# Kernel optimization log

Measured on AMD Instinct MI355X. Metric: run time of the kernel, lower is better.

## Reference

```python
import jax, jax.numpy as jnp
import numpy as np

REL_DIM = 64
HIDDEN = 128
IN_DIM = 7  # dist, dx, dy, color_diff(3), size_diff(1)


def setup_inputs() -> dict:
    key = jax.random.key(0)
    ks = jax.random.split(key, 8)
    B, N = 4, 512
    pos = jax.random.normal(ks[0], (B, N, 2), dtype=jnp.float32)
    color = jax.random.uniform(ks[1], (B, N, 3), dtype=jnp.float32)
    size = jax.random.uniform(ks[2], (B, N, 1), dtype=jnp.float32)
    # MLP params: Linear(7,128) -> GELU -> Linear(128,64), torch default init scale
    W1 = jax.random.normal(ks[3], (IN_DIM, HIDDEN), dtype=jnp.float32) / np.sqrt(IN_DIM)
    b1 = jax.random.normal(ks[4], (HIDDEN,), dtype=jnp.float32) * 0.01
    W2 = jax.random.normal(ks[5], (HIDDEN, REL_DIM), dtype=jnp.float32) / np.sqrt(HIDDEN)
    b2 = jax.random.normal(ks[6], (REL_DIM,), dtype=jnp.float32) * 0.01
    return {"pos": pos, "color": color, "size": size,
            "W1": W1, "b1": b1, "W2": W2, "b2": b2}


def reference(pos, color, size, W1, b1, W2, b2):
    # pos: (B,N,2), color: (B,N,3), size: (B,N,1)
    dx = pos[:, :, None, 0] - pos[:, None, :, 0]          # (B,N,N)
    dy = pos[:, :, None, 1] - pos[:, None, :, 1]          # (B,N,N)
    dist = jnp.sqrt(dx * dx + dy * dy + 1e-6)             # (B,N,N)
    color_diff = color[:, :, None, :] - color[:, None, :, :]  # (B,N,N,3)
    size_diff = size[:, :, None, :] - size[:, None, :, :]     # (B,N,N,1)
    geom = jnp.concatenate(
        [dist[..., None], dx[..., None], dy[..., None], color_diff, size_diff],
        axis=-1)                                          # (B,N,N,7)
    h = jax.nn.gelu(jnp.einsum('bijc,ch->bijh', geom, W1) + b1, approximate=False)
    rel = jnp.einsum('bijh,hr->bijr', h, W2) + b2          # (B,N,N,rel_dim)
    return rel
```

## Files before the change

kernel.cpp:

```cpp
#include <hip/hip_runtime.h>
#include <math.h>

#define NPTS 512
#define HID 128
#define RELD 64

typedef __attribute__((ext_vector_type(8))) short short8;
typedef __attribute__((ext_vector_type(4))) float f32x4;
typedef __attribute__((ext_vector_type(4))) int i32x4;

__global__ __launch_bounds__(256) void relgeom_mfma(
    const float* __restrict__ pos, const float* __restrict__ color,
    const float* __restrict__ size, const float* __restrict__ W1,
    const float* __restrict__ b1, const float* __restrict__ W2,
    const float* __restrict__ b2, float* __restrict__ out)
{
  __shared__ __align__(16) char lds[16384 + 4 * 4096];
  const int tid = threadIdx.x;
  const int lane = tid & 63;
  const int wid = tid >> 6;
  const int l15 = lane & 15, lq = lane >> 4, l3 = lane & 3;

#pragma unroll
  for (int n = 0; n < 32; ++n) {
    const int m = tid + 256 * n;
    const int k = m >> 6, r = m & 63;
    const __bf16 wb = (__bf16)W2[m];
    *(__bf16*)(lds + r * 256 + (((k >> 3) ^ (r & 7)) << 4) + (k & 7) * 2) = wb;
  }
  __syncthreads();

  const int pbase = (blockIdx.x * 4 + wid) * 64;
  const int t = pbase + lane;
  const int j = t & (NPTS - 1);
  const int bi = t >> 9;
  const int i = bi & (NPTS - 1);
  const int b = bi >> 9;
  const int pi = b * NPTS + i, pj = b * NPTS + j;

  const float dx = pos[pi * 2 + 0] - pos[pj * 2 + 0];
  const float dy = pos[pi * 2 + 1] - pos[pj * 2 + 1];
  const float g0 = sqrtf(fmaf(dx, dx, fmaf(dy, dy, 1e-6f)));
  const float g3 = color[pi * 3 + 0] - color[pj * 3 + 0];
  const float g4 = color[pi * 3 + 1] - color[pj * 3 + 1];
  const float g5 = color[pi * 3 + 2] - color[pj * 3 + 2];
  const float g6 = size[pi] - size[pj];

  f32x4 acc[4][4];
#pragma unroll
  for (int nt = 0; nt < 4; ++nt) {
    const float bb = b2[nt * 16 + l15];
#pragma unroll
    for (int s = 0; s < 4; ++s) acc[s][nt] = (f32x4){bb, bb, bb, bb};
  }

  char* const hbase = lds + 16384 + wid * 4096;

  for (int ks = 0; ks < 4; ++ks) {
    union { short s[32]; i32x4 v[4]; } hb;
#pragma unroll
    for (int kk = 0; kk < 32; ++kk) {
      const int k = ks * 32 + kk;
      float h = b1[k];
      h = fmaf(g0, W1[0 * HID + k], h);
      h = fmaf(dx, W1[1 * HID + k], h);
      h = fmaf(dy, W1[2 * HID + k], h);
      h = fmaf(g3, W1[3 * HID + k], h);
      h = fmaf(g4, W1[4 * HID + k], h);
      h = fmaf(g5, W1[5 * HID + k], h);
      h = fmaf(g6, W1[6 * HID + k], h);
      const float h2 = h * h;
      const float wq = fmaf(h2, -0.1029534f, -2.3022077f);
      const float ex = __builtin_amdgcn_exp2f(h * wq);
      const float gel = h * __builtin_amdgcn_rcpf(1.0f + ex);
      const __bf16 hbf = (__bf16)gel;
      hb.s[kk] = __builtin_bit_cast(short, hbf);
    }
#pragma unroll
    for (int d = 0; d < 4; ++d)
      *(i32x4*)(hbase + lane * 64 + ((d ^ l3) << 4)) = hb.v[d];

    short8 bfr[4];
#pragma unroll
    for (int nt = 0; nt < 4; ++nt) {
      const int r = nt * 16 + l15;
      bfr[nt] = *(const short8*)(lds + r * 256 + (((ks * 4 + lq) ^ (r & 7)) << 4));
    }
#pragma unroll
    for (int s = 0; s < 4; ++s) {
      const short8 af = *(const short8*)(hbase + (s * 16 + l15) * 64 + ((lq ^ l3) << 4));
#pragma unroll
      for (int nt = 0; nt < 4; ++nt)
        acc[s][nt] = __builtin_amdgcn_mfma_f32_16x16x32_bf16(af, bfr[nt], acc[s][nt], 0, 0, 0);
    }
  }

  float* const op = out + (size_t)pbase * RELD;
#pragma unroll
  for (int s = 0; s < 4; ++s)
#pragma unroll
    for (int nt = 0; nt < 4; ++nt)
#pragma unroll
      for (int ri = 0; ri < 4; ++ri)
        op[(s * 16 + lq * 4 + ri) * RELD + nt * 16 + l15] = acc[s][nt][ri];
}

extern "C" void kernel_launch(void* const* d_in, const int* in_sizes, int n_in,
                              void* d_out, int out_size, void* d_ws, size_t ws_size,
                              hipStream_t stream) {
  const float* pos   = (const float*)d_in[0];
  const float* color = (const float*)d_in[1];
  const float* size  = (const float*)d_in[2];
  const float* W1    = (const float*)d_in[3];
  const float* b1    = (const float*)d_in[4];
  const float* W2    = (const float*)d_in[5];
  const float* b2    = (const float*)d_in[6];
  float* out = (float*)d_out;

  const int B = in_sizes[0] / (NPTS * 2);
  const long long pairs = (long long)B * NPTS * NPTS;
  const int grid = (int)(pairs / 256);

  relgeom_mfma<<<grid, 256, 0, stream>>>(pos, color, size, W1, b1, W2, b2, out);
}
```

Baseline: 85.93 us.

## Factor first-layer linear terms into per-point tables precomputed in a prep kernel

The first linear layer is split algebraically: every term except the distance term is linear in per-point features, so per-point projections u_i (fp32 with bias) and u_j (bf16) are precomputed in a small prep kernel. The main kernel then forms each hidden pre-activation as u_i[k] - u_j[k] + dist*W1[0][k], which replaces seven FMAs per hidden unit with one FMA and a subtract. In exchange it adds a second launch, workspace use and per-pair table reads, and storing the u_j table in bf16 lowers precision. A fallback to the old kernel runs when the workspace is too small.

```diff
diff --git a/kernel.cpp b/kernel.cpp
--- a/kernel.cpp
+++ b/kernel.cpp
@@ -9,7 +9,121 @@
 typedef __attribute__((ext_vector_type(4))) float f32x4;
 typedef __attribute__((ext_vector_type(4))) int i32x4;
 
-__global__ __launch_bounds__(256) void relgeom_mfma(
+__global__ __launch_bounds__(256) void prep_tables(
+    const float* __restrict__ pos, const float* __restrict__ color,
+    const float* __restrict__ size, const float* __restrict__ W1,
+    const float* __restrict__ b1, float* __restrict__ ui,
+    unsigned short* __restrict__ uj)
+{
+  const int tid = blockIdx.x * blockDim.x + threadIdx.x;
+  const int k = tid & (HID - 1), p = tid >> 7;
+  float v = pos[p * 2 + 0] * W1[1 * HID + k];
+  v = fmaf(pos[p * 2 + 1], W1[2 * HID + k], v);
+  v = fmaf(color[p * 3 + 0], W1[3 * HID + k], v);
+  v = fmaf(color[p * 3 + 1], W1[4 * HID + k], v);
+  v = fmaf(color[p * 3 + 2], W1[5 * HID + k], v);
+  v = fmaf(size[p], W1[6 * HID + k], v);
+  ui[tid] = v + b1[k];
+  const __bf16 vb = (__bf16)v;
+  uj[tid] = __builtin_bit_cast(unsigned short, vb);
+}
+
+__global__ __launch_bounds__(256) void relgeom_mfma2(
+    const float* __restrict__ pos, const float* __restrict__ W1,
+    const float* __restrict__ ui, const unsigned short* __restrict__ uj,
+    const float* __restrict__ W2, const float* __restrict__ b2,
+    float* __restrict__ out)
+{
+  __shared__ __align__(16) char lds[16384 + 4 * 4096];
+  const int tid = threadIdx.x;
+  const int lane = tid & 63;
+  const int wid = tid >> 6;
+  const int l15 = lane & 15, lq = lane >> 4, l3 = lane & 3;
+
+#pragma unroll
+  for (int n = 0; n < 32; ++n) {
+    const int m = tid + 256 * n;
+    const int k = m >> 6, r = m & 63;
+    const __bf16 wb = (__bf16)W2[m];
+    *(__bf16*)(lds + r * 256 + (((k >> 3) ^ (r & 7)) << 4) + (k & 7) * 2) = wb;
+  }
+  __syncthreads();
+
+  const int pbase = (blockIdx.x * 4 + wid) * 64;
+  const int t = pbase + lane;
+  const int j = t & (NPTS - 1);
+  const int bi = t >> 9;
+  const int i = bi & (NPTS - 1);
+  const int b = bi >> 9;
+  const int pi = b * NPTS + i, pj = b * NPTS + j;
+
+  const float dx = pos[pi * 2 + 0] - pos[pj * 2 + 0];
+  const float dy = pos[pi * 2 + 1] - pos[pj * 2 + 1];
+  const float dist = sqrtf(fmaf(dx, dx, fmaf(dy, dy, 1e-6f)));
+
+  const float* __restrict__ uirow = ui + (size_t)pi * HID;
+  const unsigned short* __restrict__ ujrow = uj + (size_t)pj * HID;
+
+  f32x4 acc[4][4];
+#pragma unroll
+  for (int nt = 0; nt < 4; ++nt) {
+    const float bb = b2[nt * 16 + l15];
+#pragma unroll
+    for (int s = 0; s < 4; ++s) acc[s][nt] = (f32x4){bb, bb, bb, bb};
+  }
+
+  char* const hbase = lds + 16384 + wid * 4096;
+
+  for (int ks = 0; ks < 4; ++ks) {
+    union { i32x4 v[4]; unsigned u[16]; } U;
+#pragma unroll
+    for (int d = 0; d < 4; ++d)
+      U.v[d] = *(const i32x4*)(ujrow + ks * 32 + d * 8);
+
+    union { short s[32]; i32x4 v[4]; } hb;
+#pragma unroll
+    for (int kk = 0; kk < 32; ++kk) {
+      const int k = ks * 32 + kk;
+      const unsigned w = U.u[kk >> 1];
+      const float ujf = __builtin_bit_cast(float, (kk & 1) ? (w & 0xffff0000u) : (w << 16));
+      float h = fmaf(dist, W1[k], uirow[k] - ujf);
+      const float h2 = h * h;
+      const float wq = fmaf(h2, -0.1029534f, -2.3022077f);
+      const float ex = __builtin_amdgcn_exp2f(h * wq);
+      const float gel = h * __builtin_amdgcn_rcpf(1.0f + ex);
+      const __bf16 hbf = (__bf16)gel;
+      hb.s[kk] = __builtin_bit_cast(short, hbf);
+    }
+#pragma unroll
+    for (int d = 0; d < 4; ++d)
+      *(i32x4*)(hbase + lane * 64 + ((d ^ l3) << 4)) = hb.v[d];
+
+    short8 bfr[4];
+#pragma unroll
+    for (int nt = 0; nt < 4; ++nt) {
+      const int r = nt * 16 + l15;
+      bfr[nt] = *(const short8*)(lds + r * 256 + (((ks * 4 + lq) ^ (r & 7)) << 4));
+    }
+#pragma unroll
+    for (int s = 0; s < 4; ++s) {
+      const short8 af = *(const short8*)(hbase + (s * 16 + l15) * 64 + ((lq ^ l3) << 4));
+#pragma unroll
+      for (int nt = 0; nt < 4; ++nt)
+        acc[s][nt] = __builtin_amdgcn_mfma_f32_16x16x32_bf16(af, bfr[nt], acc[s][nt], 0, 0, 0);
+    }
+  }
+
+  float* const op = out + (size_t)pbase * RELD;
+#pragma unroll
+  for (int s = 0; s < 4; ++s)
+#pragma unroll
+    for (int nt = 0; nt < 4; ++nt)
+#pragma unroll
+      for (int ri = 0; ri < 4; ++ri)
+        op[(s * 16 + lq * 4 + ri) * RELD + nt * 16 + l15] = acc[s][nt][ri];
+}
+
+__global__ __launch_bounds__(256) void relgeom_mfma_fb(
     const float* __restrict__ pos, const float* __restrict__ color,
     const float* __restrict__ size, const float* __restrict__ W1,
     const float* __restrict__ b1, const float* __restrict__ W2,
@@ -20,7 +134,6 @@
   const int lane = tid & 63;
   const int wid = tid >> 6;
   const int l15 = lane & 15, lq = lane >> 4, l3 = lane & 3;
-
 #pragma unroll
   for (int n = 0; n < 32; ++n) {
     const int m = tid + 256 * n;
@@ -29,7 +142,6 @@
     *(__bf16*)(lds + r * 256 + (((k >> 3) ^ (r & 7)) << 4) + (k & 7) * 2) = wb;
   }
   __syncthreads();
-
   const int pbase = (blockIdx.x * 4 + wid) * 64;
   const int t = pbase + lane;
   const int j = t & (NPTS - 1);
@@ -37,7 +149,6 @@
   const int i = bi & (NPTS - 1);
   const int b = bi >> 9;
   const int pi = b * NPTS + i, pj = b * NPTS + j;
-
   const float dx = pos[pi * 2 + 0] - pos[pj * 2 + 0];
   const float dy = pos[pi * 2 + 1] - pos[pj * 2 + 1];
   const float g0 = sqrtf(fmaf(dx, dx, fmaf(dy, dy, 1e-6f)));
@@ -45,7 +156,6 @@
   const float g4 = color[pi * 3 + 1] - color[pj * 3 + 1];
   const float g5 = color[pi * 3 + 2] - color[pj * 3 + 2];
   const float g6 = size[pi] - size[pj];
-
   f32x4 acc[4][4];
 #pragma unroll
   for (int nt = 0; nt < 4; ++nt) {
@@ -53,9 +163,7 @@
 #pragma unroll
     for (int s = 0; s < 4; ++s) acc[s][nt] = (f32x4){bb, bb, bb, bb};
   }
-
   char* const hbase = lds + 16384 + wid * 4096;
-
   for (int ks = 0; ks < 4; ++ks) {
     union { short s[32]; i32x4 v[4]; } hb;
 #pragma unroll
@@ -79,7 +187,6 @@
 #pragma unroll
     for (int d = 0; d < 4; ++d)
       *(i32x4*)(hbase + lane * 64 + ((d ^ l3) << 4)) = hb.v[d];
-
     short8 bfr[4];
 #pragma unroll
     for (int nt = 0; nt < 4; ++nt) {
@@ -94,7 +201,6 @@
         acc[s][nt] = __builtin_amdgcn_mfma_f32_16x16x32_bf16(af, bfr[nt], acc[s][nt], 0, 0, 0);
     }
   }
-
   float* const op = out + (size_t)pbase * RELD;
 #pragma unroll
   for (int s = 0; s < 4; ++s)
@@ -118,8 +224,19 @@
   float* out = (float*)d_out;
 
   const int B = in_sizes[0] / (NPTS * 2);
+  const int npts = B * NPTS;
   const long long pairs = (long long)B * NPTS * NPTS;
   const int grid = (int)(pairs / 256);
 
-  relgeom_mfma<<<grid, 256, 0, stream>>>(pos, color, size, W1, b1, W2, b2, out);
-}
+  const size_t ui_bytes = (size_t)npts * HID * sizeof(float);
+  const size_t uj_bytes = (size_t)npts * HID * sizeof(unsigned short);
+
+  if (ws_size >= ui_bytes + uj_bytes) {
+    float* ui = (float*)d_ws;
+    unsigned short* uj = (unsigned short*)((char*)d_ws + ui_bytes);
+    prep_tables<<<npts * HID / 256, 256, 0, stream>>>(pos, color, size, W1, b1, ui, uj);
+    relgeom_mfma2<<<grid, 256, 0, stream>>>(pos, W1, ui, uj, W2, b2, out);
+  } else {
+    relgeom_mfma_fb<<<grid, 256, 0, stream>>>(pos, color, size, W1, b1, W2, b2, out);
+  }
+}
```

New measurement: 108.7 us. 26.6% more time.
